# Performance work log

Measured on AMD Instinct MI355X. Metric: run time of the kernel, lower is better.

## Reference

```python
import jax, jax.numpy as jnp
import numpy as np

N_NODES = 100000
N_EDGES = 1600000
IN_C = 128
OUT_C = 64
EDGE_DIM = 32
BN_EPS = 1e-5


def setup_inputs() -> dict:
    key = jax.random.key(0)
    ks = jax.random.split(key, 10)
    s = lambda fan_in: 1.0 / np.sqrt(fan_in)
    return {
        "x": jax.random.normal(ks[0], (N_NODES, IN_C), jnp.float32),
        "edge_index": jax.random.randint(ks[1], (2, N_EDGES), 0, N_NODES, jnp.int64),
        "edge_attr": jax.random.normal(ks[2], (N_EDGES, EDGE_DIM), jnp.float32),
        # SAGEConv params: lin_l (neighbors, with bias), lin_r (root, no bias)
        "W_l": jax.random.uniform(ks[3], (IN_C, OUT_C), jnp.float32, -s(IN_C), s(IN_C)),
        "b_l": jnp.zeros((OUT_C,), jnp.float32),
        "W_r": jax.random.uniform(ks[4], (IN_C, OUT_C), jnp.float32, -s(IN_C), s(IN_C)),
        # edge_transform: Linear(EDGE_DIM, OUT_C)
        "W_e": jax.random.uniform(ks[5], (EDGE_DIM, OUT_C), jnp.float32, -s(EDGE_DIM), s(EDGE_DIM)),
        "b_e": jax.random.uniform(ks[6], (OUT_C,), jnp.float32, -s(EDGE_DIM), s(EDGE_DIM)),
        # gate: Linear(2*OUT_C, OUT_C)
        "W_g": jax.random.uniform(ks[7], (2 * OUT_C, OUT_C), jnp.float32, -s(2 * OUT_C), s(2 * OUT_C)),
        "b_g": jax.random.uniform(ks[8], (OUT_C,), jnp.float32, -s(2 * OUT_C), s(2 * OUT_C)),
        # BatchNorm1d affine params
        "gamma": jnp.ones((OUT_C,), jnp.float32),
        "beta": jnp.zeros((OUT_C,), jnp.float32),
    }


def reference(x, edge_index, edge_attr, W_l, b_l, W_r, W_e, b_e, W_g, b_g, gamma, beta):
    n = x.shape[0]
    row, col = edge_index[0], edge_index[1]  # source, target

    # --- SAGEConv (mean aggregation): agg[i] = mean_{e: col[e]==i} x[row[e]]
    agg = jax.ops.segment_sum(x[row], col, num_segments=n)  # [N, IN_C]
    cnt = jax.ops.segment_sum(jnp.ones((row.shape[0],), x.dtype), col, num_segments=n)
    agg = agg / jnp.maximum(cnt, 1.0)[:, None]
    out = agg @ W_l + b_l + x @ W_r  # [N, OUT_C]

    # --- edge gating
    ea = edge_attr @ W_e + b_e  # [E, OUT_C]
    combined = jnp.concatenate([out[col], ea], axis=-1)  # [E, 2*OUT_C]
    gate = jax.nn.sigmoid(combined @ W_g + b_g)  # [E, OUT_C]
    contrib = gate * ea  # [E, OUT_C]
    out = out + jax.ops.segment_sum(contrib, col, num_segments=n)

    # --- BatchNorm1d (training: batch stats, biased variance)
    mu = jnp.mean(out, axis=0)
    var = jnp.mean(jnp.square(out - mu), axis=0)
    out = gamma * (out - mu) * jax.lax.rsqrt(var + BN_EPS) + beta

    # residual = Identity -> out + out, then ReLU
    return jax.nn.relu(2.0 * out)
```

## Files before the change

### kernel.cpp

```cpp
#include <hip/hip_runtime.h>
#include <math.h>

#define NN 100000
#define NE 1600000
#define INC 128
#define OC 64
#define ED 32

typedef __attribute__((ext_vector_type(8))) short bf16x8;
typedef __attribute__((ext_vector_type(4))) float f32x4;

__device__ __forceinline__ float sigmoidf_(float z) {
    return __builtin_amdgcn_rcpf(1.0f + __expf(-z));
}

__device__ __forceinline__ unsigned short f2bf(float x) {
    unsigned int u = __float_as_uint(x);
    unsigned int r = u + 0x7FFFu + ((u >> 16) & 1u);
    return (unsigned short)(r >> 16);
}
__device__ __forceinline__ float bf2f(unsigned short u) {
    return __uint_as_float((unsigned int)u << 16);
}
__device__ __forceinline__ unsigned cvtpk(float lo, float hi) {
    unsigned r;
    asm("v_cvt_pk_bf16_f32 %0, %1, %2" : "=v"(r) : "v"(lo), "v"(hi));
    return r;
}

extern "C" __global__ void __launch_bounds__(256)
k_wfuse(const float* __restrict__ We, const float* __restrict__ be,
        const float* __restrict__ Wg, const float* __restrict__ Wl,
        const float* __restrict__ Wr, unsigned short* __restrict__ WfT,
        unsigned short* __restrict__ WeT, float* __restrict__ hb,
        unsigned short* __restrict__ WlrT) {
    int idx = blockIdx.x * 256 + threadIdx.x;
    if (idx < ED * OC) {
        int ch = idx >> 5, d = idx & 31;
        float acc = 0.0f;
#pragma unroll
        for (int k = 0; k < OC; ++k)
            acc = fmaf(We[d * OC + k], Wg[(OC + k) * OC + ch], acc);
        WfT[idx] = f2bf(acc);
    } else if (idx < 2 * ED * OC) {
        int i2 = idx - ED * OC;
        int ch = i2 >> 5, d = i2 & 31;
        WeT[i2] = f2bf(We[d * OC + ch]);
    } else if (idx < 2 * ED * OC + OC) {
        int j = idx - 2 * ED * OC;
        float acc = 0.0f;
#pragma unroll
        for (int k = 0; k < OC; ++k)
            acc = fmaf(be[k], Wg[(OC + k) * OC + j], acc);
        hb[j] = acc;
    } else if (idx < 2 * ED * OC + OC + 2 * INC * OC) {
        int i3 = idx - (2 * ED * OC + OC);
        int ch = i3 >> 7, k = i3 & 127;
        float v = (ch < OC) ? Wl[k * OC + ch] : Wr[k * OC + (ch - OC)];
        WlrT[i3] = f2bf(v);
    }
}

extern "C" __global__ void __launch_bounds__(256)
k_xw(const float* __restrict__ x, const unsigned short* __restrict__ WlrT,
     unsigned short* __restrict__ ybf, unsigned short* __restrict__ xwrbf,
     const int* __restrict__ colv, int* __restrict__ cnti) {
    int t = threadIdx.x;
    {
        int eb = (blockIdx.x * 256 + t) * 4;
        if (eb + 3 < NE) {
            int4 cv = *reinterpret_cast<const int4*>(colv + eb);
            int c0 = min(max(cv.x, 0), NN - 1);
            int c1 = min(max(cv.y, 0), NN - 1);
            int c2 = min(max(cv.z, 0), NN - 1);
            int c3 = min(max(cv.w, 0), NN - 1);
            atomicAdd(&cnti[c0], 1);
            atomicAdd(&cnti[c1], 1);
            atomicAdd(&cnti[c2], 1);
            atomicAdd(&cnti[c3], 1);
        }
    }

    __shared__ unsigned short xs[64][136];
    int base = blockIdx.x * 64;
    {
        int rr = t >> 2, cc = (t & 3) * 32;
        int grow = base + rr;
        if (grow < NN) {
            const float4* xp = reinterpret_cast<const float4*>(
                x + (size_t)grow * INC + cc);
#pragma unroll
            for (int q = 0; q < 8; ++q) {
                float4 v = xp[q];
                uint2 uv;
                uv.x = cvtpk(v.x, v.y);
                uv.y = cvtpk(v.z, v.w);
                *reinterpret_cast<uint2*>(&xs[rr][cc + q * 4]) = uv;
            }
        } else {
#pragma unroll
            for (int q = 0; q < 8; ++q) {
                uint2 uv; uv.x = 0u; uv.y = 0u;
                *reinterpret_cast<uint2*>(&xs[rr][cc + q * 4]) = uv;
            }
        }
    }
    __syncthreads();

    int lane = t & 63, w = t >> 6;
    int c = lane & 15, g = lane >> 4;

    bf16x8 bw0[4], bw1[4];
#pragma unroll
    for (int kk = 0; kk < 4; ++kk) {
        bw0[kk] = *reinterpret_cast<const bf16x8*>(
            WlrT + (w * 32 + 0 * 16 + c) * INC + kk * 32 + g * 8);
        bw1[kk] = *reinterpret_cast<const bf16x8*>(
            WlrT + (w * 32 + 1 * 16 + c) * INC + kk * 32 + g * 8);
    }

    f32x4 acc[4][2];
#pragma unroll
    for (int mt = 0; mt < 4; ++mt)
#pragma unroll
        for (int nt = 0; nt < 2; ++nt)
            acc[mt][nt] = (f32x4){0.0f, 0.0f, 0.0f, 0.0f};

#pragma unroll
    for (int kk = 0; kk < 4; ++kk) {
        bf16x8 a0 = *reinterpret_cast<const bf16x8*>(&xs[0 * 16 + c][kk * 32 + g * 8]);
        bf16x8 a1 = *reinterpret_cast<const bf16x8*>(&xs[1 * 16 + c][kk * 32 + g * 8]);
        bf16x8 a2 = *reinterpret_cast<const bf16x8*>(&xs[2 * 16 + c][kk * 32 + g * 8]);
        bf16x8 a3 = *reinterpret_cast<const bf16x8*>(&xs[3 * 16 + c][kk * 32 + g * 8]);
        acc[0][0] = __builtin_amdgcn_mfma_f32_16x16x32_bf16(a0, bw0[kk], acc[0][0], 0, 0, 0);
        acc[0][1] = __builtin_amdgcn_mfma_f32_16x16x32_bf16(a0, bw1[kk], acc[0][1], 0, 0, 0);
        acc[1][0] = __builtin_amdgcn_mfma_f32_16x16x32_bf16(a1, bw0[kk], acc[1][0], 0, 0, 0);
        acc[1][1] = __builtin_amdgcn_mfma_f32_16x16x32_bf16(a1, bw1[kk], acc[1][1], 0, 0, 0);
        acc[2][0] = __builtin_amdgcn_mfma_f32_16x16x32_bf16(a2, bw0[kk], acc[2][0], 0, 0, 0);
        acc[2][1] = __builtin_amdgcn_mfma_f32_16x16x32_bf16(a2, bw1[kk], acc[2][1], 0, 0, 0);
        acc[3][0] = __builtin_amdgcn_mfma_f32_16x16x32_bf16(a3, bw0[kk], acc[3][0], 0, 0, 0);
        acc[3][1] = __builtin_amdgcn_mfma_f32_16x16x32_bf16(a3, bw1[kk], acc[3][1], 0, 0, 0);
    }

#pragma unroll
    for (int mt = 0; mt < 4; ++mt) {
#pragma unroll
        for (int nt = 0; nt < 2; ++nt) {
            int ch = w * 32 + nt * 16 + c;
#pragma unroll
            for (int j = 0; j < 4; ++j) {
                int row = base + mt * 16 + g * 4 + j;
                if (row < NN) {
                    unsigned short vb = f2bf(acc[mt][nt][j]);
                    if (ch < OC) ybf[(size_t)row * OC + ch] = vb;
                    else         xwrbf[(size_t)row * OC + (ch - OC)] = vb;
                }
            }
        }
    }
}

extern "C" __global__ void __launch_bounds__(1024)
k_scanA(const int* __restrict__ cnti, int* __restrict__ cur,
        int* __restrict__ bsum) {
    __shared__ int s[1024];
    int t = threadIdx.x;
    int idx = blockIdx.x * 1024 + t;
    int v = (idx < NN) ? cnti[idx] : 0;
    s[t] = v;
    __syncthreads();
#pragma unroll
    for (int off = 1; off < 1024; off <<= 1) {
        int tmp = (t >= off) ? s[t - off] : 0;
        __syncthreads();
        s[t] += tmp;
        __syncthreads();
    }
    if (idx < NN) cur[idx] = s[t] - v;
    if (t == 1023) bsum[blockIdx.x] = s[1023];
}

extern "C" __global__ void __launch_bounds__(128)
k_scanB(int* __restrict__ bsum) {
    __shared__ int s[128];
    int t = threadIdx.x;
    int v = (t < 98) ? bsum[t] : 0;
    s[t] = v;
    __syncthreads();
#pragma unroll
    for (int off = 1; off < 128; off <<= 1) {
        int tmp = (t >= off) ? s[t - off] : 0;
        __syncthreads();
        s[t] += tmp;
        __syncthreads();
    }
    if (t < 98) bsum[t] = s[t] - v;
}

extern "C" __global__ void __launch_bounds__(1024)
k_scanC(int* __restrict__ cur, const int* __restrict__ bsum) {
    int idx = blockIdx.x * 1024 + threadIdx.x;
    if (idx < NN) cur[idx] += bsum[blockIdx.x];
}

extern "C" __global__ void __launch_bounds__(256)
k_bucket(const int* __restrict__ colv, const int* __restrict__ rowv,
         int* __restrict__ cur, unsigned long long* __restrict__ ec) {
    int eb = (blockIdx.x * 256 + threadIdx.x) * 4;
    if (eb >= NE) return;
    int4 cv = *reinterpret_cast<const int4*>(colv + eb);
    int4 rv = *reinterpret_cast<const int4*>(rowv + eb);
    int c0 = min(max(cv.x, 0), NN - 1), r0 = min(max(rv.x, 0), NN - 1);
    int c1 = min(max(cv.y, 0), NN - 1), r1 = min(max(rv.y, 0), NN - 1);
    int c2 = min(max(cv.z, 0), NN - 1), r2 = min(max(rv.z, 0), NN - 1);
    int c3 = min(max(cv.w, 0), NN - 1), r3 = min(max(rv.w, 0), NN - 1);
    int p0 = atomicAdd(&cur[c0], 1);
    int p1 = atomicAdd(&cur[c1], 1);
    int p2 = atomicAdd(&cur[c2], 1);
    int p3 = atomicAdd(&cur[c3], 1);
    ec[p0] = ((unsigned long long)(unsigned)r0 << 47) |
             ((unsigned long long)(unsigned)c0 << 30) | (unsigned)(eb + 0);
    ec[p1] = ((unsigned long long)(unsigned)r1 << 47) |
             ((unsigned long long)(unsigned)c1 << 30) | (unsigned)(eb + 1);
    ec[p2] = ((unsigned long long)(unsigned)r2 << 47) |
             ((unsigned long long)(unsigned)c2 << 30) | (unsigned)(eb + 2);
    ec[p3] = ((unsigned long long)(unsigned)r3 << 47) |
             ((unsigned long long)(unsigned)c3 << 30) | (unsigned)(eb + 3);
}

extern "C" __global__ void __launch_bounds__(256)
k_aggoh(const unsigned long long* __restrict__ ec, const int* __restrict__ cur,
        const unsigned short* __restrict__ ybf, unsigned short* xwr_h,
        const float* __restrict__ bl, const float* __restrict__ Wg,
        const float* __restrict__ bg, const float* __restrict__ hb,
        float* __restrict__ agg) {
    __shared__ float ol[4][64];
    int w = threadIdx.x >> 6, c = threadIdx.x & 63;
    int i = blockIdx.x * 4 + w;
    if (i >= NN) return;
    int start = (i == 0) ? 0 : cur[i - 1];
    int end = cur[i];
    float xwr = bf2f(xwr_h[(size_t)i * OC + c]);
    float acc = 0.0f;
    int p = start;
    for (; p + 7 < end; p += 8) {
        int r0 = (int)(ec[p + 0] >> 47);
        int r1 = (int)(ec[p + 1] >> 47);
        int r2 = (int)(ec[p + 2] >> 47);
        int r3 = (int)(ec[p + 3] >> 47);
        int r4 = (int)(ec[p + 4] >> 47);
        int r5 = (int)(ec[p + 5] >> 47);
        int r6 = (int)(ec[p + 6] >> 47);
        int r7 = (int)(ec[p + 7] >> 47);
        unsigned short u0 = ybf[(size_t)r0 * OC + c];
        unsigned short u1 = ybf[(size_t)r1 * OC + c];
        unsigned short u2 = ybf[(size_t)r2 * OC + c];
        unsigned short u3 = ybf[(size_t)r3 * OC + c];
        unsigned short u4 = ybf[(size_t)r4 * OC + c];
        unsigned short u5 = ybf[(size_t)r5 * OC + c];
        unsigned short u6 = ybf[(size_t)r6 * OC + c];
        unsigned short u7 = ybf[(size_t)r7 * OC + c];
        acc += bf2f(u0); acc += bf2f(u1); acc += bf2f(u2); acc += bf2f(u3);
        acc += bf2f(u4); acc += bf2f(u5); acc += bf2f(u6); acc += bf2f(u7);
    }
    for (; p < end; ++p) {
        int r0 = (int)(ec[p] >> 47);
        acc += bf2f(ybf[(size_t)r0 * OC + c]);
    }
    float inv = 1.0f / fmaxf((float)(end - start), 1.0f);
    float o = fmaf(acc, inv, bl[c] + xwr);
    agg[(size_t)i * OC + c] = o;
    ol[w][c] = o;
    __builtin_amdgcn_wave_barrier();
    float h0 = bg[c] + hb[c];
    float h1 = 0.0f, h2 = 0.0f, h3 = 0.0f;
#pragma unroll
    for (int k = 0; k < OC; k += 4) {
        float o0 = ol[w][k + 0], o1 = ol[w][k + 1];
        float o2 = ol[w][k + 2], o3 = ol[w][k + 3];
        h0 = fmaf(o0, Wg[(k + 0) * OC + c], h0);
        h1 = fmaf(o1, Wg[(k + 1) * OC + c], h1);
        h2 = fmaf(o2, Wg[(k + 2) * OC + c], h2);
        h3 = fmaf(o3, Wg[(k + 3) * OC + c], h3);
    }
    float h = (h0 + h1) + (h2 + h3);
    xwr_h[(size_t)i * OC + (c & 15) * 4 + (c >> 4)] = f2bf(h);
}

extern "C" __global__ void __launch_bounds__(256, 3)
k_gate_ns(const unsigned long long* __restrict__ ec, const float* __restrict__ eattr,
          const unsigned short* __restrict__ WfT, const unsigned short* __restrict__ WeT,
          const float* __restrict__ be, const unsigned short* __restrict__ hswz,
          unsigned short* __restrict__ contrib) {
    int lane = threadIdx.x & 63;
    int w = threadIdx.x >> 6;
    int tb = (blockIdx.x * 4 + w) * 64;

    unsigned long long ev = ec[tb + lane];
    int e = (int)(ev & 0x3FFFFFFFULL);
    int cl = (int)((ev >> 30) & 0x1FFFFULL);
    int c = lane & 15, g = lane >> 4;

    int erow0 = __shfl(e, 0 * 16 + c);
    int erow1 = __shfl(e, 1 * 16 + c);
    int erow2 = __shfl(e, 2 * 16 + c);
    int erow3 = __shfl(e, 3 * 16 + c);
    int clx[16];
#pragma unroll
    for (int mt = 0; mt < 4; ++mt)
#pragma unroll
        for (int r = 0; r < 4; ++r)
            clx[mt * 4 + r] = __shfl(cl, mt * 16 + g * 4 + r);

    uint2 hg[16];
#pragma unroll
    for (int q = 0; q < 16; ++q)
        hg[q] = *reinterpret_cast<const uint2*>(hswz + (size_t)clx[q] * OC + c * 4);

    bf16x8 bwf[4], bwe[4];
    float bev[4];
#pragma unroll
    for (int nt = 0; nt < 4; ++nt) {
        int ch = nt * 16 + c;
        bwf[nt] = *reinterpret_cast<const bf16x8*>(WfT + ch * ED + g * 8);
        bwe[nt] = *reinterpret_cast<const bf16x8*>(WeT + ch * ED + g * 8);
        bev[nt] = be[ch];
    }

    float4 alo0 = reinterpret_cast<const float4*>(eattr + (size_t)erow0 * ED + g * 8)[0];
    float4 ahi0 = reinterpret_cast<const float4*>(eattr + (size_t)erow0 * ED + g * 8)[1];
    float4 alo1 = reinterpret_cast<const float4*>(eattr + (size_t)erow1 * ED + g * 8)[0];
    float4 ahi1 = reinterpret_cast<const float4*>(eattr + (size_t)erow1 * ED + g * 8)[1];
    float4 alo2 = reinterpret_cast<const float4*>(eattr + (size_t)erow2 * ED + g * 8)[0];
    float4 ahi2 = reinterpret_cast<const float4*>(eattr + (size_t)erow2 * ED + g * 8)[1];
    float4 alo3 = reinterpret_cast<const float4*>(eattr + (size_t)erow3 * ED + g * 8)[0];
    float4 ahi3 = reinterpret_cast<const float4*>(eattr + (size_t)erow3 * ED + g * 8)[1];

    bf16x8 afr[4];
    {
        union { bf16x8 v; unsigned d[4]; } pk;
#define PACKA(idx, lo, hi)                         \
        pk.d[0] = cvtpk(lo.x, lo.y);               \
        pk.d[1] = cvtpk(lo.z, lo.w);               \
        pk.d[2] = cvtpk(hi.x, hi.y);               \
        pk.d[3] = cvtpk(hi.z, hi.w);               \
        afr[idx] = pk.v;
        PACKA(0, alo0, ahi0)
        PACKA(1, alo1, ahi1)
        PACKA(2, alo2, ahi2)
        PACKA(3, alo3, ahi3)
#undef PACKA
    }

#pragma unroll
    for (int mt = 0; mt < 4; ++mt) {
        uint2 h0 = hg[mt * 4 + 0];
        uint2 h1 = hg[mt * 4 + 1];
        uint2 h2 = hg[mt * 4 + 2];
        uint2 h3 = hg[mt * 4 + 3];
        float sv[4][4];
#pragma unroll
        for (int nt = 0; nt < 4; ++nt) {
            f32x4 cz, ce;
            unsigned w0 = (nt < 2) ? h0.x : h0.y;
            unsigned w1 = (nt < 2) ? h1.x : h1.y;
            unsigned w2 = (nt < 2) ? h2.x : h2.y;
            unsigned w3 = (nt < 2) ? h3.x : h3.y;
            cz[0] = bf2f((unsigned short)((nt & 1) ? (w0 >> 16) : (w0 & 0xffffu)));
            cz[1] = bf2f((unsigned short)((nt & 1) ? (w1 >> 16) : (w1 & 0xffffu)));
            cz[2] = bf2f((unsigned short)((nt & 1) ? (w2 >> 16) : (w2 & 0xffffu)));
            cz[3] = bf2f((unsigned short)((nt & 1) ? (w3 >> 16) : (w3 & 0xffffu)));
            ce[0] = bev[nt]; ce[1] = bev[nt]; ce[2] = bev[nt]; ce[3] = bev[nt];
            f32x4 z  = __builtin_amdgcn_mfma_f32_16x16x32_bf16(afr[mt], bwf[nt], cz, 0, 0, 0);
            f32x4 ea = __builtin_amdgcn_mfma_f32_16x16x32_bf16(afr[mt], bwe[nt], ce, 0, 0, 0);
            sv[nt][0] = sigmoidf_(z[0]) * ea[0];
            sv[nt][1] = sigmoidf_(z[1]) * ea[1];
            sv[nt][2] = sigmoidf_(z[2]) * ea[2];
            sv[nt][3] = sigmoidf_(z[3]) * ea[3];
        }
#pragma unroll
        for (int r = 0; r < 4; ++r) {
            int row = tb + mt * 16 + g * 4 + r;
            uint2 pk;
            pk.x = cvtpk(sv[0][r], sv[1][r]);
            pk.y = cvtpk(sv[2][r], sv[3][r]);
            *reinterpret_cast<uint2*>(contrib + (size_t)row * OC + c * 4) = pk;
        }
    }
}

extern "C" __global__ void __launch_bounds__(256, 3)
k_gate_at(const unsigned long long* __restrict__ ec, const float* __restrict__ eattr,
          const unsigned short* __restrict__ WfT, const unsigned short* __restrict__ WeT,
          const float* __restrict__ be, const unsigned short* __restrict__ hswz,
          float* __restrict__ agg) {
    int lane = threadIdx.x & 63;
    int w = threadIdx.x >> 6;
    int tb = (blockIdx.x * 4 + w) * 64;

    unsigned long long ev = ec[tb + lane];
    int e = (int)(ev & 0x3FFFFFFFULL);
    int cl = (int)((ev >> 30) & 0x1FFFFULL);
    int c = lane & 15, g = lane >> 4;

    int erow0 = __shfl(e, 0 * 16 + c);
    int erow1 = __shfl(e, 1 * 16 + c);
    int erow2 = __shfl(e, 2 * 16 + c);
    int erow3 = __shfl(e, 3 * 16 + c);
    int clx[16];
#pragma unroll
    for (int mt = 0; mt < 4; ++mt)
#pragma unroll
        for (int r = 0; r < 4; ++r)
            clx[mt * 4 + r] = __shfl(cl, mt * 16 + g * 4 + r);

    uint2 hg[16];
#pragma unroll
    for (int q = 0; q < 16; ++q)
        hg[q] = *reinterpret_cast<const uint2*>(hswz + (size_t)clx[q] * OC + c * 4);

    bf16x8 bwf[4], bwe[4];
    float bev[4];
#pragma unroll
    for (int nt = 0; nt < 4; ++nt) {
        int ch = nt * 16 + c;
        bwf[nt] = *reinterpret_cast<const bf16x8*>(WfT + ch * ED + g * 8);
        bwe[nt] = *reinterpret_cast<const bf16x8*>(WeT + ch * ED + g * 8);
        bev[nt] = be[ch];
    }

    float4 alo0 = reinterpret_cast<const float4*>(eattr + (size_t)erow0 * ED + g * 8)[0];
    float4 ahi0 = reinterpret_cast<const float4*>(eattr + (size_t)erow0 * ED + g * 8)[1];
    float4 alo1 = reinterpret_cast<const float4*>(eattr + (size_t)erow1 * ED + g * 8)[0];
    float4 ahi1 = reinterpret_cast<const float4*>(eattr + (size_t)erow1 * ED + g * 8)[1];
    float4 alo2 = reinterpret_cast<const float4*>(eattr + (size_t)erow2 * ED + g * 8)[0];
    float4 ahi2 = reinterpret_cast<const float4*>(eattr + (size_t)erow2 * ED + g * 8)[1];
    float4 alo3 = reinterpret_cast<const float4*>(eattr + (size_t)erow3 * ED + g * 8)[0];
    float4 ahi3 = reinterpret_cast<const float4*>(eattr + (size_t)erow3 * ED + g * 8)[1];

    bf16x8 afr[4];
    {
        union { bf16x8 v; unsigned d[4]; } pk;
#define PACKA(idx, lo, hi)                         \
        pk.d[0] = cvtpk(lo.x, lo.y);               \
        pk.d[1] = cvtpk(lo.z, lo.w);               \
        pk.d[2] = cvtpk(hi.x, hi.y);               \
        pk.d[3] = cvtpk(hi.z, hi.w);               \
        afr[idx] = pk.v;
        PACKA(0, alo0, ahi0)
        PACKA(1, alo1, ahi1)
        PACKA(2, alo2, ahi2)
        PACKA(3, alo3, ahi3)
#undef PACKA
    }

#pragma unroll
    for (int mt = 0; mt < 4; ++mt) {
        int cl0 = clx[mt * 4 + 0];
        int cl1 = clx[mt * 4 + 1];
        int cl2 = clx[mt * 4 + 2];
        int cl3 = clx[mt * 4 + 3];
        uint2 h0 = hg[mt * 4 + 0];
        uint2 h1 = hg[mt * 4 + 1];
        uint2 h2 = hg[mt * 4 + 2];
        uint2 h3 = hg[mt * 4 + 3];
#pragma unroll
        for (int nt = 0; nt < 4; ++nt) {
            int ch = nt * 16 + c;
            f32x4 cz, ce;
            unsigned w0 = (nt < 2) ? h0.x : h0.y;
            unsigned w1 = (nt < 2) ? h1.x : h1.y;
            unsigned w2 = (nt < 2) ? h2.x : h2.y;
            unsigned w3 = (nt < 2) ? h3.x : h3.y;
            cz[0] = bf2f((unsigned short)((nt & 1) ? (w0 >> 16) : (w0 & 0xffffu)));
            cz[1] = bf2f((unsigned short)((nt & 1) ? (w1 >> 16) : (w1 & 0xffffu)));
            cz[2] = bf2f((unsigned short)((nt & 1) ? (w2 >> 16) : (w2 & 0xffffu)));
            cz[3] = bf2f((unsigned short)((nt & 1) ? (w3 >> 16) : (w3 & 0xffffu)));
            ce[0] = bev[nt]; ce[1] = bev[nt]; ce[2] = bev[nt]; ce[3] = bev[nt];
            f32x4 z  = __builtin_amdgcn_mfma_f32_16x16x32_bf16(afr[mt], bwf[nt], cz, 0, 0, 0);
            f32x4 ea = __builtin_amdgcn_mfma_f32_16x16x32_bf16(afr[mt], bwe[nt], ce, 0, 0, 0);
            float c0 = sigmoidf_(z[0]) * ea[0];
            float c1 = sigmoidf_(z[1]) * ea[1];
            float c2 = sigmoidf_(z[2]) * ea[2];
            float c3 = sigmoidf_(z[3]) * ea[3];
            float s = c0;
            int t = cl0;
            if (cl1 != t) { atomicAdd(&agg[(size_t)t * OC + ch], s); s = 0.0f; t = cl1; }
            s += c1;
            if (cl2 != t) { atomicAdd(&agg[(size_t)t * OC + ch], s); s = 0.0f; t = cl2; }
            s += c2;
            if (cl3 != t) { atomicAdd(&agg[(size_t)t * OC + ch], s); s = 0.0f; t = cl3; }
            s += c3;
            atomicAdd(&agg[(size_t)t * OC + ch], s);
        }
    }
}

extern "C" __global__ void __launch_bounds__(256)
k_csumst(const unsigned short* __restrict__ contrib, const int* __restrict__ cur,
         float* __restrict__ agg, float* __restrict__ stats) {
    __shared__ float ls[256], lq[256];
    int w = threadIdx.x >> 6, c = threadIdx.x & 63;
    int ch = (c >> 2) + 16 * (c & 3);
    float sv = 0.0f, sq = 0.0f;
    for (int i = blockIdx.x * 4 + w; i < NN; i += 2048 * 4) {
        int start = (i == 0) ? 0 : cur[i - 1];
        int end = cur[i];
        float s = 0.0f;
        int p = start;
        for (; p + 7 < end; p += 8) {
            unsigned short u0 = contrib[(size_t)(p + 0) * OC + c];
            unsigned short u1 = contrib[(size_t)(p + 1) * OC + c];
            unsigned short u2 = contrib[(size_t)(p + 2) * OC + c];
            unsigned short u3 = contrib[(size_t)(p + 3) * OC + c];
            unsigned short u4 = contrib[(size_t)(p + 4) * OC + c];
            unsigned short u5 = contrib[(size_t)(p + 5) * OC + c];
            unsigned short u6 = contrib[(size_t)(p + 6) * OC + c];
            unsigned short u7 = contrib[(size_t)(p + 7) * OC + c];
            s += bf2f(u0); s += bf2f(u1); s += bf2f(u2); s += bf2f(u3);
            s += bf2f(u4); s += bf2f(u5); s += bf2f(u6); s += bf2f(u7);
        }
        for (; p < end; ++p) s += bf2f(contrib[(size_t)p * OC + c]);
        float v = agg[(size_t)i * OC + ch] + s;
        agg[(size_t)i * OC + ch] = v;
        sv += v;
        sq = fmaf(v, v, sq);
    }
    ls[threadIdx.x] = sv;
    lq[threadIdx.x] = sq;
    __syncthreads();
    if (threadIdx.x < 64) {
        float a = ls[c] + ls[c + 64] + ls[c + 128] + ls[c + 192];
        float b = lq[c] + lq[c + 64] + lq[c + 128] + lq[c + 192];
        atomicAdd(&stats[ch], a);
        atomicAdd(&stats[OC + ch], b);
    }
}

extern "C" __global__ void __launch_bounds__(256)
k_stats(const float* __restrict__ a, float* __restrict__ stats) {
    __shared__ float ls[256], lq[256];
    int t = threadIdx.x;
    float s = 0.0f, q = 0.0f;
    for (size_t idx = (size_t)blockIdx.x * 256 + t; idx < (size_t)NN * OC;
         idx += (size_t)gridDim.x * 256) {
        float v = a[idx];
        s += v;
        q = fmaf(v, v, q);
    }
    ls[t] = s; lq[t] = q;
    __syncthreads();
    if (t < OC) {
        s = ls[t] + ls[t + 64] + ls[t + 128] + ls[t + 192];
        q = lq[t] + lq[t + 64] + lq[t + 128] + lq[t + 192];
        atomicAdd(&stats[t], s);
        atomicAdd(&stats[OC + t], q);
    }
}

extern "C" __global__ void __launch_bounds__(256)
k_final(const float* __restrict__ a, const float* __restrict__ stats,
        const float* __restrict__ gamma, const float* __restrict__ beta,
        float* __restrict__ out) {
    size_t idx = (size_t)blockIdx.x * 256 + threadIdx.x;
    if (idx >= (size_t)NN * OC) return;
    int c = (int)(idx & 63);
    float mu = stats[c] * (1.0f / NN);
    float var = stats[OC + c] * (1.0f / NN) - mu * mu;
    float v = a[idx];
    float y = fmaf(gamma[c] * (v - mu), rsqrtf(var + 1e-5f), beta[c]);
    out[idx] = fmaxf(2.0f * y, 0.0f);
}

extern "C" void kernel_launch(void* const* d_in, const int* in_sizes, int n_in,
                              void* d_out, int out_size, void* d_ws, size_t ws_size,
                              hipStream_t stream) {
    const float* x     = (const float*)d_in[0];
    const int*   ei    = (const int*)d_in[1];
    const float* eattr = (const float*)d_in[2];
    const float* Wl    = (const float*)d_in[3];
    const float* bl    = (const float*)d_in[4];
    const float* Wr    = (const float*)d_in[5];
    const float* We    = (const float*)d_in[6];
    const float* be    = (const float*)d_in[7];
    const float* Wg    = (const float*)d_in[8];
    const float* bg    = (const float*)d_in[9];
    const float* gamma = (const float*)d_in[10];
    const float* beta  = (const float*)d_in[11];
    float* out = (float*)d_out;

    float* agg = (float*)d_ws;
    unsigned short* ybf   = (unsigned short*)(agg + (size_t)NN * OC);
    unsigned short* xwrbf = ybf + (size_t)NN * OC;
    unsigned long long* ec = (unsigned long long*)(xwrbf + (size_t)NN * OC);
    int* cur   = (int*)(ec + (size_t)NE);
    int* bsum  = cur + NN;
    float* stats = (float*)(bsum + 128);
    unsigned short* WfT  = (unsigned short*)(stats + 128);
    unsigned short* WeT  = WfT + ED * OC;
    unsigned short* WlrT = WeT + ED * OC;
    float* hb = (float*)(WlrT + 2 * INC * OC);
    unsigned short* contrib = (unsigned short*)(hb + OC);
    unsigned short* hswz = xwrbf;

    size_t base_bytes = (size_t)((char*)(hb + OC) - (char*)d_ws);
    bool ns = ws_size >= base_bytes + (size_t)NE * OC * sizeof(unsigned short);

    const int* rowv = ei;
    const int* colv = ei + NE;

    hipMemsetAsync(cur, 0, NN * sizeof(int), stream);
    hipMemsetAsync(stats, 0, 2 * OC * sizeof(float), stream);

    k_wfuse<<<(2 * ED * OC + OC + 2 * INC * OC + 255) / 256, 256, 0, stream>>>(
        We, be, Wg, Wl, Wr, WfT, WeT, hb, WlrT);
    k_xw<<<(NN + 63) / 64, 256, 0, stream>>>(x, WlrT, ybf, xwrbf, colv, cur);
    k_scanA<<<98, 1024, 0, stream>>>(cur, cur, bsum);
    k_scanB<<<1, 128, 0, stream>>>(bsum);
    k_scanC<<<98, 1024, 0, stream>>>(cur, bsum);
    k_bucket<<<(NE / 4 + 255) / 256, 256, 0, stream>>>(colv, rowv, cur, ec);
    k_aggoh<<<(NN + 3) / 4, 256, 0, stream>>>(ec, cur, ybf, xwrbf, bl, Wg, bg, hb, agg);
    if (ns) {
        k_gate_ns<<<NE / 256, 256, 0, stream>>>(ec, eattr, WfT, WeT, be, hswz, contrib);
        k_csumst<<<2048, 256, 0, stream>>>(contrib, cur, agg, stats);
    } else {
        k_gate_at<<<NE / 256, 256, 0, stream>>>(ec, eattr, WfT, WeT, be, hswz, agg);
        k_stats<<<2048, 256, 0, stream>>>(agg, stats);
    }
    k_final<<<((size_t)NN * OC + 255) / 256, 256, 0, stream>>>(agg, stats, gamma, beta, out);
}
```

Before: 548.6 us.

## Replace single-pass edge bucketing with two-pass coarse/fine radix scatter

Edge bucketing by target node becomes two passes. A coarse pass bins edges into 256 ranges of 512 nodes, using shared-memory histograms and one global atomic per bin per block, and writes them to a staging buffer. A fine pass then scatters each edge to its exact CSR slot. The aim is better locality for the per-node atomics and scattered 8-byte writes, at the cost of an extra read/write pass over 1.6M edges and two more launches; the staging buffer aliases the contrib workspace, which is only written later.

```diff
diff --git a/kernel.cpp b/kernel.cpp
--- a/kernel.cpp
+++ b/kernel.cpp
@@ -26,6 +26,11 @@
     unsigned r;
     asm("v_cvt_pk_bf16_f32 %0, %1, %2" : "=v"(r) : "v"(lo), "v"(hi));
     return r;
+}
+
+__device__ __forceinline__ unsigned long long pack_ec(int r, int cl, int e) {
+    return ((unsigned long long)(unsigned)r << 47) |
+           ((unsigned long long)(unsigned)cl << 30) | (unsigned)e;
 }
 
 extern "C" __global__ void __launch_bounds__(256)
@@ -204,28 +209,88 @@
 }
 
 extern "C" __global__ void __launch_bounds__(256)
+k_init256(const int* __restrict__ cur, int* __restrict__ gcur256) {
+    int t = threadIdx.x;
+    int nb = t * 512;
+    gcur256[t] = (nb < NN) ? cur[nb] : NE;
+}
+
+extern "C" __global__ void __launch_bounds__(256)
+k_coarse(const int* __restrict__ colv, const int* __restrict__ rowv,
+         int* __restrict__ gcur256, unsigned long long* __restrict__ ecp) {
+    __shared__ int lh[256];
+    __shared__ int sbase[256];
+    int t = threadIdx.x;
+    lh[t] = 0;
+    __syncthreads();
+    int e0 = blockIdx.x * 2048 + t * 8;
+    int cls[8], rws[8];
+    if (e0 + 7 < NE) {
+        int4 a = *reinterpret_cast<const int4*>(colv + e0);
+        int4 b = *reinterpret_cast<const int4*>(colv + e0 + 4);
+        int4 ra = *reinterpret_cast<const int4*>(rowv + e0);
+        int4 rb = *reinterpret_cast<const int4*>(rowv + e0 + 4);
+        cls[0] = a.x; cls[1] = a.y; cls[2] = a.z; cls[3] = a.w;
+        cls[4] = b.x; cls[5] = b.y; cls[6] = b.z; cls[7] = b.w;
+        rws[0] = ra.x; rws[1] = ra.y; rws[2] = ra.z; rws[3] = ra.w;
+        rws[4] = rb.x; rws[5] = rb.y; rws[6] = rb.z; rws[7] = rb.w;
+    } else {
+#pragma unroll
+        for (int j = 0; j < 8; ++j) {
+            cls[j] = (e0 + j < NE) ? colv[e0 + j] : 0;
+            rws[j] = (e0 + j < NE) ? rowv[e0 + j] : 0;
+        }
+    }
+    int d[8];
+#pragma unroll
+    for (int j = 0; j < 8; ++j) {
+        if (e0 + j < NE) {
+            cls[j] = min(max(cls[j], 0), NN - 1);
+            rws[j] = min(max(rws[j], 0), NN - 1);
+            d[j] = cls[j] >> 9;
+            atomicAdd(&lh[d[j]], 1);
+        } else {
+            d[j] = -1;
+        }
+    }
+    __syncthreads();
+    int cnt = lh[t];
+    if (cnt) sbase[t] = atomicAdd(&gcur256[t], cnt);
+    __syncthreads();
+    lh[t] = 0;
+    __syncthreads();
+#pragma unroll
+    for (int j = 0; j < 8; ++j) {
+        if (d[j] >= 0) {
+            int r = atomicAdd(&lh[d[j]], 1);
+            ecp[sbase[d[j]] + r] = pack_ec(rws[j], cls[j], e0 + j);
+        }
+    }
+}
+
+extern "C" __global__ void __launch_bounds__(256)
+k_fine(const unsigned long long* __restrict__ ecp, int* __restrict__ cur,
+       unsigned long long* __restrict__ ec) {
+    int p = blockIdx.x * 256 + threadIdx.x;
+    if (p >= NE) return;
+    unsigned long long v = ecp[p];
+    int cl = (int)((v >> 30) & 0x1FFFFULL);
+    cl = min(cl, NN - 1);
+    int pos = atomicAdd(&cur[cl], 1);
+    ec[pos] = v;
+}
+
+extern "C" __global__ void __launch_bounds__(256)
 k_bucket(const int* __restrict__ colv, const int* __restrict__ rowv,
          int* __restrict__ cur, unsigned long long* __restrict__ ec) {
-    int eb = (blockIdx.x * 256 + threadIdx.x) * 4;
-    if (eb >= NE) return;
-    int4 cv = *reinterpret_cast<const int4*>(colv + eb);
-    int4 rv = *reinterpret_cast<const int4*>(rowv + eb);
-    int c0 = min(max(cv.x, 0), NN - 1), r0 = min(max(rv.x, 0), NN - 1);
-    int c1 = min(max(cv.y, 0), NN - 1), r1 = min(max(rv.y, 0), NN - 1);
-    int c2 = min(max(cv.z, 0), NN - 1), r2 = min(max(rv.z, 0), NN - 1);
-    int c3 = min(max(cv.w, 0), NN - 1), r3 = min(max(rv.w, 0), NN - 1);
-    int p0 = atomicAdd(&cur[c0], 1);
-    int p1 = atomicAdd(&cur[c1], 1);
-    int p2 = atomicAdd(&cur[c2], 1);
-    int p3 = atomicAdd(&cur[c3], 1);
-    ec[p0] = ((unsigned long long)(unsigned)r0 << 47) |
-             ((unsigned long long)(unsigned)c0 << 30) | (unsigned)(eb + 0);
-    ec[p1] = ((unsigned long long)(unsigned)r1 << 47) |
-             ((unsigned long long)(unsigned)c1 << 30) | (unsigned)(eb + 1);
-    ec[p2] = ((unsigned long long)(unsigned)r2 << 47) |
-             ((unsigned long long)(unsigned)c2 << 30) | (unsigned)(eb + 2);
-    ec[p3] = ((unsigned long long)(unsigned)r3 << 47) |
-             ((unsigned long long)(unsigned)c3 << 30) | (unsigned)(eb + 3);
+    int e = blockIdx.x * 256 + threadIdx.x;
+    if (e >= NE) return;
+    int cl = colv[e];
+    cl = min(max(cl, 0), NN - 1);
+    int r = rowv[e];
+    r = min(max(r, 0), NN - 1);
+    int pos = atomicAdd(&cur[cl], 1);
+    ec[pos] = pack_ec(r, cl, e);
 }
 
 extern "C" __global__ void __launch_bounds__(256)
@@ -600,11 +665,14 @@
     unsigned short* WeT  = WfT + ED * OC;
     unsigned short* WlrT = WeT + ED * OC;
     float* hb = (float*)(WlrT + 2 * INC * OC);
-    unsigned short* contrib = (unsigned short*)(hb + OC);
+    int* gcur256 = (int*)(hb + OC);
+    unsigned short* contrib = (unsigned short*)(gcur256 + 256);
+    unsigned long long* ecp =
+        (unsigned long long*)(((size_t)contrib + 7) & ~(size_t)7);
     unsigned short* hswz = xwrbf;
 
-    size_t base_bytes = (size_t)((char*)(hb + OC) - (char*)d_ws);
-    bool ns = ws_size >= base_bytes + (size_t)NE * OC * sizeof(unsigned short);
+    size_t base_bytes = (size_t)((char*)contrib - (char*)d_ws);
+    bool ns = ws_size >= base_bytes + 8 + (size_t)NE * OC * sizeof(unsigned short);
 
     const int* rowv = ei;
     const int* colv = ei + NE;
@@ -618,7 +686,13 @@
     k_scanA<<<98, 1024, 0, stream>>>(cur, cur, bsum);
     k_scanB<<<1, 128, 0, stream>>>(bsum);
     k_scanC<<<98, 1024, 0, stream>>>(cur, bsum);
-    k_bucket<<<(NE / 4 + 255) / 256, 256, 0, stream>>>(colv, rowv, cur, ec);
+    if (ns) {
+        k_init256<<<1, 256, 0, stream>>>(cur, gcur256);
+        k_coarse<<<(NE + 2047) / 2048, 256, 0, stream>>>(colv, rowv, gcur256, ecp);
+        k_fine<<<(NE + 255) / 256, 256, 0, stream>>>(ecp, cur, ec);
+    } else {
+        k_bucket<<<(NE + 255) / 256, 256, 0, stream>>>(colv, rowv, cur, ec);
+    }
     k_aggoh<<<(NN + 3) / 4, 256, 0, stream>>>(ec, cur, ybf, xwrbf, bl, Wg, bg, hb, agg);
     if (ns) {
         k_gate_ns<<<NE / 256, 256, 0, stream>>>(ec, eattr, WfT, WeT, be, hswz, contrib);
```

Measured after the change: 471.7 us (median of 2 runs). 1.16x faster.
